# Performance work log

Hardware: AMD Instinct MI355X
Metric: run time of the kernel (lower is better)

Reference implementation:

```python
import jax, jax.numpy as jnp
import numpy as np

NUM_HEADS = 4
KERNEL = 4
EPS = 1e-6


def _causal_conv1d(x, w, b):
    # x: (B,S,D), w: (D,1,K) depthwise, b: (D,)
    xc = x.transpose(0, 2, 1)  # (B,D,S)
    y = jax.lax.conv_general_dilated(
        xc, w, window_strides=(1,), padding=[(w.shape[-1] - 1, 0)],
        feature_group_count=xc.shape[1])
    return (y + b[None, :, None]).transpose(0, 2, 1)  # (B,S,D)


def _headwise(x, w):
    # x: (B,S,D), w: (NH, DH_out, DH_in) block-diagonal linear, no bias
    B, S, D = x.shape
    nh, dout, din = w.shape
    xh = x.reshape(B, S, nh, din)
    return jnp.einsum('bshd,hod->bsho', xh, w).reshape(B, S, nh * dout)


def _slstm_scan(gates, R, b):
    # gates: (B,S,4,NH,DH) ordered [i,f,z,o]; R: (NH,DH,4*DH); b: (4,NH,DH)
    B, S, _, nh, dh = gates.shape
    gseq = gates.transpose(1, 0, 2, 3, 4)  # (S,B,4,NH,DH)
    zero = jnp.zeros((B, nh, dh), gates.dtype)
    init = (zero, zero, zero, zero)  # h, c, n, m

    def step(carry, g):
        h, c, n, m = carry
        rec = jnp.einsum('bhd,hdk->bhk', h, R)
        rec = rec.reshape(B, nh, 4, dh).transpose(0, 2, 1, 3)  # (B,4,NH,DH)
        raw = g + rec + b[None]
        iraw, fraw, zraw, oraw = raw[:, 0], raw[:, 1], raw[:, 2], raw[:, 3]
        logfplusm = m + jax.nn.log_sigmoid(fraw)
        m_new = jnp.maximum(iraw, logfplusm)  # stabilizer
        ig = jnp.exp(iraw - m_new)
        fg = jnp.exp(logfplusm - m_new)
        c_new = fg * c + ig * jnp.tanh(zraw)
        n_new = fg * n + ig
        h_new = jax.nn.sigmoid(oraw) * c_new / n_new
        return (h_new, c_new, n_new, m_new), h_new

    _, ys = jax.lax.scan(step, init, gseq)  # ys: (S,B,NH,DH)
    return ys.transpose(1, 2, 0, 3)  # (B,NH,S,DH)


def _multihead_layernorm(y, scale, bias):
    # y: (B,NH,S,DH); normalize over DH per head
    mu = y.mean(-1, keepdims=True)
    var = y.var(-1, keepdims=True)
    yn = (y - mu) * jax.lax.rsqrt(var + EPS)
    nh, dh = y.shape[1], y.shape[3]
    return yn * scale.reshape(1, nh, 1, dh) + bias.reshape(1, nh, 1, dh)


def setup_inputs() -> dict:
    key = jax.random.key(0)
    ks = jax.random.split(key, 12)
    B, S, D = 4, 2048, 1024
    nh, dh = NUM_HEADS, D // NUM_HEADS
    sd_conv = 1.0 / np.sqrt(KERNEL)
    sd_head = 1.0 / np.sqrt(dh)
    return {
        'x': jax.random.normal(ks[0], (B, S, D), jnp.float32),
        'conv_w': jax.random.normal(ks[1], (D, 1, KERNEL), jnp.float32) * sd_conv,
        'conv_b': jnp.zeros((D,), jnp.float32),
        'w_i': jax.random.normal(ks[2], (nh, dh, dh), jnp.float32) * sd_head,
        'w_f': jax.random.normal(ks[3], (nh, dh, dh), jnp.float32) * sd_head,
        'w_z': jax.random.normal(ks[4], (nh, dh, dh), jnp.float32) * sd_head,
        'w_o': jax.random.normal(ks[5], (nh, dh, dh), jnp.float32) * sd_head,
        'rec_kernel': jax.random.normal(ks[6], (nh, dh, 4 * dh), jnp.float32) * sd_head,
        'cell_bias': jnp.zeros((4, nh, dh), jnp.float32),
        'gn_scale': jnp.ones((D,), jnp.float32),
        'gn_bias': jnp.zeros((D,), jnp.float32),
    }


def reference(x, conv_w, conv_b, w_i, w_f, w_z, w_o, rec_kernel, cell_bias, gn_scale, gn_bias):
    B, S, D = x.shape
    dh = D // NUM_HEADS
    x_conv = jax.nn.swish(_causal_conv1d(x, conv_w, conv_b))
    i = _headwise(x_conv, w_i)
    f = _headwise(x_conv, w_f)
    z = _headwise(x, w_z)
    o = _headwise(x, w_o)
    # concat order [i,f,z,o]; reshape to (B,S,4,NH,DH)
    gates = jnp.stack([i, f, z, o], axis=2).reshape(B, S, 4, NUM_HEADS, dh)
    y = _slstm_scan(gates, rec_kernel, cell_bias)  # (B,NH,S,DH)
    out = _multihead_layernorm(y, gn_scale, gn_bias)
    return out.transpose(0, 2, 1, 3).reshape(B, S, D)
```

## Files before the change

### kernel.cpp

```cpp
#include <hip/hip_runtime.h>
#include <hip/hip_bf16.h>

#define NH 4
#define DH 256
#define DMODEL 1024
#define BB 4
#define SS 2048

typedef __attribute__((ext_vector_type(4))) float f32x4;
typedef __attribute__((ext_vector_type(8))) short bf16x8;
typedef __attribute__((ext_vector_type(4))) int i32x4;

__device__ __forceinline__ int dot4i8(int acc, int a, int b) {
#if __has_builtin(__builtin_amdgcn_sdot4)
    return __builtin_amdgcn_sdot4(a, b, acc, false);
#else
#pragma unroll
    for (int i = 0; i < 4; ++i) {
        int av = (a << (24 - 8 * i)) >> 24;
        int bv = (b << (24 - 8 * i)) >> 24;
        acc += av * bv;
    }
    return acc;
#endif
}

__device__ __forceinline__ void wg_barrier() {
    asm volatile("s_waitcnt lgkmcnt(0)" ::: "memory");
    __builtin_amdgcn_s_barrier();
}

__device__ __forceinline__ float xor1_f32(float v) {
    int r = __builtin_amdgcn_update_dpp(0, __float_as_int(v), 0xB1, 0xF, 0xF, true);
    return __int_as_float(r);
}

__global__ void k_conv(const float* __restrict__ x, const float* __restrict__ cw,
                       const float* __restrict__ cb, float* __restrict__ xc) {
    int bs = blockIdx.x;
    int s = bs & (SS - 1);
    const float* xrow = x + (size_t)bs * DMODEL;
#pragma unroll
    for (int dd = 0; dd < 4; ++dd) {
        int d = threadIdx.x + dd * 256;
        float w0 = cw[d * 4 + 0], w1 = cw[d * 4 + 1], w2 = cw[d * 4 + 2], w3 = cw[d * 4 + 3];
        float acc = cb[d] + w3 * xrow[d];
        if (s >= 1) acc += w2 * xrow[d - DMODEL];
        if (s >= 2) acc += w1 * xrow[d - 2 * DMODEL];
        if (s >= 3) acc += w0 * xrow[d - 3 * DMODEL];
        float sig = 1.f / (1.f + __expf(-acc));
        xc[(size_t)bs * DMODEL + d] = acc * sig;
    }
}

__global__ void k_gemm(const float* __restrict__ x, const float* __restrict__ xc,
                       const float* __restrict__ wi, const float* __restrict__ wf,
                       const float* __restrict__ wz, const float* __restrict__ wo,
                       float* __restrict__ gates) {
    int h = blockIdx.z >> 1, pair = blockIdx.z & 1;
    const float* A = pair ? x : xc;
    int n0 = blockIdx.y * 64;
    const float* W = (n0 < 256) ? (pair ? wz : wi) : (pair ? wo : wf);
    int nl = n0 & 255;
    int m0 = blockIdx.x * 64;

    __shared__ __align__(16) __hip_bfloat16 Al[64][72];
    __shared__ __align__(16) __hip_bfloat16 Bl[64][72];

    int tid = threadIdx.x;
    int lane = tid & 63, wv = tid >> 6;
    f32x4 acc[4] = {};

    for (int k0 = 0; k0 < 256; k0 += 64) {
        __syncthreads();
#pragma unroll
        for (int i = 0; i < 4; ++i) {
            int f4 = tid + i * 256;
            int r = f4 >> 4, c4 = (f4 & 15) * 4;
            const float* srcA = A + (size_t)(m0 + r) * DMODEL + h * DH + k0 + c4;
            float4 v = *(const float4*)srcA;
            Al[r][c4 + 0] = __float2bfloat16(v.x);
            Al[r][c4 + 1] = __float2bfloat16(v.y);
            Al[r][c4 + 2] = __float2bfloat16(v.z);
            Al[r][c4 + 3] = __float2bfloat16(v.w);
            const float* srcB = W + (size_t)(h * DH + nl + r) * DH + k0 + c4;
            float4 u = *(const float4*)srcB;
            Bl[r][c4 + 0] = __float2bfloat16(u.x);
            Bl[r][c4 + 1] = __float2bfloat16(u.y);
            Bl[r][c4 + 2] = __float2bfloat16(u.z);
            Bl[r][c4 + 3] = __float2bfloat16(u.w);
        }
        __syncthreads();
#pragma unroll
        for (int kk = 0; kk < 64; kk += 32) {
            bf16x8 a = *(const bf16x8*)&Al[wv * 16 + (lane & 15)][kk + (lane >> 4) * 8];
#pragma unroll
            for (int nt = 0; nt < 4; ++nt) {
                bf16x8 bfr = *(const bf16x8*)&Bl[nt * 16 + (lane & 15)][kk + (lane >> 4) * 8];
                acc[nt] = __builtin_amdgcn_mfma_f32_16x16x32_bf16(a, bfr, acc[nt], 0, 0, 0);
            }
        }
    }
#pragma unroll
    for (int nt = 0; nt < 4; ++nt)
#pragma unroll
        for (int r = 0; r < 4; ++r) {
            int m = m0 + wv * 16 + (lane >> 4) * 4 + r;
            int n = n0 + nt * 16 + (lane & 15);
            int b = m >> 11, s = m & (SS - 1);
            int g = pair * 2 + (n >> 8), d = n & 255;
            gates[((((size_t)(b * NH + h)) * SS + s) * 4 + g) * DH + d] = acc[nt][r];
        }
}

__global__ void k_prep(const float* __restrict__ R, int* __restrict__ Wq,
                       float* __restrict__ scales) {
    int colid = blockIdx.x * 4 + (threadIdx.x >> 6);
    int lane = threadIdx.x & 63;
    int h = colid >> 10, k = colid & 1023;
    const float* base = R + (size_t)h * 256 * 1024 + k;
    float v[4];
    float mx = 0.f;
#pragma unroll
    for (int i = 0; i < 4; ++i) {
        v[i] = base[(size_t)(lane * 4 + i) * 1024];
        mx = fmaxf(mx, fabsf(v[i]));
    }
    for (int off = 32; off; off >>= 1) mx = fmaxf(mx, __shfl_xor(mx, off));
    mx = fmaxf(mx, 1e-30f);
    float scale = mx * (1.f / 127.f);
    float inv = 127.f / mx;
    int pk = 0;
#pragma unroll
    for (int i = 0; i < 4; ++i) {
        int q = (int)rintf(v[i] * inv);
        q = max(-127, min(127, q));
        pk |= (q & 255) << (8 * i);
    }
    Wq[(h * 64 + lane) * 1024 + k] = pk;
    if (lane == 0) scales[h * 1024 + k] = scale;
}

__launch_bounds__(512, 2)
__global__ void k_scan(const float* __restrict__ gates, const int* __restrict__ Wq,
                       const float* __restrict__ scales, const float* __restrict__ bias,
                       float* __restrict__ y) {
    int bh = blockIdx.x;
    int h = bh & 3;
    int t = threadIdx.x;
    int d = t >> 1, pair = t & 1;

    __shared__ __align__(16) signed char hq[2][256];

    int col0 = pair * 256 + d;
    int col1 = col0 + 512;

    int w0[64], w1[64];
#pragma unroll
    for (int j = 0; j < 64; ++j) {
        w0[j] = Wq[(h * 64 + j) * 1024 + col0];
        w1[j] = Wq[(h * 64 + j) * 1024 + col1];
    }
    float cm0 = scales[h * 1024 + col0] * (1.f / 127.f);
    float cm1 = scales[h * 1024 + col1] * (1.f / 127.f);
    float b0 = bias[(pair * NH + h) * DH + d];
    float b1 = bias[((2 + pair) * NH + h) * DH + d];

    float c = 0.f, n = 0.f, mstate = 0.f;
    const float* gbase = gates + (size_t)bh * SS * 1024;
    float* ybase = y + (size_t)bh * SS * DH + d;

    if (t < 32) ((i32x4*)hq)[t] = (i32x4){0, 0, 0, 0};
    __syncthreads();

    float gA0 = gbase[col0], gA1 = gbase[col1];
    float gB0 = gbase[1024 + col0], gB1 = gbase[1024 + col1];

#define SCAN_STEP(P, G0, G1, SCUR)                                            \
    {                                                                          \
        int acc0 = 0, acc1 = 0;                                                \
        const i32x4* hv4 = (const i32x4*)hq[P];                                \
        _Pragma("unroll") for (int kb = 0; kb < 4; ++kb) {                     \
            i32x4 ha = hv4[kb * 4 + 0];                                        \
            i32x4 hb = hv4[kb * 4 + 1];                                        \
            i32x4 hc = hv4[kb * 4 + 2];                                        \
            i32x4 hd_ = hv4[kb * 4 + 3];                                       \
            int hd[16] = {ha.x, ha.y, ha.z, ha.w, hb.x, hb.y, hb.z, hb.w,      \
                          hc.x, hc.y, hc.z, hc.w, hd_.x, hd_.y, hd_.z, hd_.w}; \
            _Pragma("unroll") for (int j = 0; j < 16; ++j) {                   \
                acc0 = dot4i8(acc0, w0[kb * 16 + j], hd[j]);                   \
                acc1 = dot4i8(acc1, w1[kb * 16 + j], hd[j]);                   \
            }                                                                  \
        }                                                                      \
        float rawA = G0 + (float)acc0 * cm0 + b0;                              \
        float rawB = G1 + (float)acc1 * cm1 + b1;                              \
        int sp = (SCUR) + 2 < SS ? (SCUR) + 2 : SS - 1;                        \
        G0 = gbase[(size_t)sp * 1024 + col0];                                  \
        G1 = gbase[(size_t)sp * 1024 + col1];                                  \
        float recvA = xor1_f32(rawA);                                          \
        float recvB = xor1_f32(rawB);                                          \
        float rawi = pair ? recvA : rawA;                                      \
        float rawf = pair ? rawA : recvA;                                      \
        float rawz = pair ? recvB : rawB;                                      \
        float rawo = pair ? rawB : recvB;                                      \
        float lsf = fminf(rawf, 0.f) - __logf(1.f + __expf(-fabsf(rawf)));     \
        float lfm = mstate + lsf;                                              \
        float mn = fmaxf(rawi, lfm);                                           \
        float ig = __expf(rawi - mn);                                          \
        float fg = __expf(lfm - mn);                                           \
        float az = fabsf(rawz);                                                \
        float e2 = __expf(-2.f * az);                                          \
        float th = (1.f - e2) / (1.f + e2);                                    \
        th = rawz < 0.f ? -th : th;                                            \
        c = fg * c + ig * th;                                                  \
        n = fg * n + ig;                                                       \
        mstate = mn;                                                           \
        float so = 1.f / (1.f + __expf(-rawo));                                \
        float hv = so * c / n;                                                 \
        if (!pair) {                                                           \
            ybase[(size_t)(SCUR)*DH] = hv;                                     \
            hq[(P) ^ 1][d] = (signed char)(int)rintf(hv * 127.f);              \
        }                                                                      \
        wg_barrier();                                                          \
    }

    for (int s = 0; s < SS; s += 2) {
        SCAN_STEP(0, gA0, gA1, s)
        SCAN_STEP(1, gB0, gB1, s + 1)
    }
#undef SCAN_STEP
}

__global__ void k_ln(const float* __restrict__ y, const float* __restrict__ gsc,
                     const float* __restrict__ gbi, float* __restrict__ out) {
    int bid = blockIdx.x;
    int s = bid & (SS - 1);
    int bh = bid >> 11;
    int b = bh >> 2, h = bh & 3;
    int d = threadIdx.x;
    float v = y[(size_t)bid * DH + d];
    float s1 = v, s2 = v * v;
    for (int off = 32; off; off >>= 1) {
        s1 += __shfl_xor(s1, off);
        s2 += __shfl_xor(s2, off);
    }
    __shared__ float a1[4], a2[4];
    int wv = threadIdx.x >> 6, ln = threadIdx.x & 63;
    if (ln == 0) { a1[wv] = s1; a2[wv] = s2; }
    __syncthreads();
    s1 = a1[0] + a1[1] + a1[2] + a1[3];
    s2 = a2[0] + a2[1] + a2[2] + a2[3];
    float mu = s1 * (1.f / 256.f);
    float var = s2 * (1.f / 256.f) - mu * mu;
    float rs = rsqrtf(var + 1e-6f);
    float o = (v - mu) * rs * gsc[h * DH + d] + gbi[h * DH + d];
    out[((size_t)(b * SS + s)) * DMODEL + h * DH + d] = o;
}

extern "C" void kernel_launch(void* const* d_in, const int* in_sizes, int n_in,
                              void* d_out, int out_size, void* d_ws, size_t ws_size,
                              hipStream_t stream) {
    (void)in_sizes; (void)n_in; (void)out_size; (void)ws_size;
    const float* x = (const float*)d_in[0];
    const float* cw = (const float*)d_in[1];
    const float* cb = (const float*)d_in[2];
    const float* wi = (const float*)d_in[3];
    const float* wf = (const float*)d_in[4];
    const float* wz = (const float*)d_in[5];
    const float* wo = (const float*)d_in[6];
    const float* R = (const float*)d_in[7];
    const float* cbias = (const float*)d_in[8];
    const float* gsc = (const float*)d_in[9];
    const float* gbi = (const float*)d_in[10];
    float* out = (float*)d_out;

    char* ws = (char*)d_ws;
    float* xc = (float*)ws;
    float* gates = (float*)(ws + 33554432ull);
    float* yb = (float*)(ws + 167772160ull);
    int* Wq = (int*)(ws + 201326592ull);
    float* scales = (float*)(ws + 202375168ull);

    k_prep<<<1024, 256, 0, stream>>>(R, Wq, scales);
    k_conv<<<BB * SS, 256, 0, stream>>>(x, cw, cb, xc);
    k_gemm<<<dim3(128, 8, 8), 256, 0, stream>>>(x, xc, wi, wf, wz, wo, gates);
    k_scan<<<16, 512, 0, stream>>>(gates, Wq, scales, cbias, yb);
    k_ln<<<BB * SS * NH, 256, 0, stream>>>(yb, gsc, gbi, out);
}
```

Measured before the change: 2.136 ms.

## Split scan recurrence between MFMA for input gate and sdot4 for others

The scan kernel moves from 512 threads (two per hidden unit, exchanging gate values via DPP) to 256 threads, one per hidden unit. The input-gate recurrent matvec now runs on the int8 MFMA unit with its result broadcast by lane shuffles, while the forget, z and output gates stay on scalar sdot4 loops held in registers. The aim is to overlap matrix-core and VALU work inside each sequential step and drop the pair exchange. The cost is higher register pressure per thread and a heavier VALU chain per lane, which could lengthen each step.

```diff
diff --git a/kernel.cpp b/kernel.cpp
--- a/kernel.cpp
+++ b/kernel.cpp
@@ -28,11 +28,7 @@
 __device__ __forceinline__ void wg_barrier() {
     asm volatile("s_waitcnt lgkmcnt(0)" ::: "memory");
     __builtin_amdgcn_s_barrier();
-}
-
-__device__ __forceinline__ float xor1_f32(float v) {
-    int r = __builtin_amdgcn_update_dpp(0, __float_as_int(v), 0xB1, 0xF, 0xF, true);
-    return __int_as_float(r);
+    __builtin_amdgcn_sched_barrier(0);
 }
 
 __global__ void k_conv(const float* __restrict__ x, const float* __restrict__ cw,
@@ -141,94 +137,137 @@
     if (lane == 0) scales[h * 1024 + k] = scale;
 }
 
-__launch_bounds__(512, 2)
+__launch_bounds__(256, 1)
 __global__ void k_scan(const float* __restrict__ gates, const int* __restrict__ Wq,
                        const float* __restrict__ scales, const float* __restrict__ bias,
                        float* __restrict__ y) {
     int bh = blockIdx.x;
     int h = bh & 3;
-    int t = threadIdx.x;
-    int d = t >> 1, pair = t & 1;
+    int d = threadIdx.x;
+    int lane = d & 63;
+    int wv = d >> 6;
+    int kg = lane >> 4;
+    int cl = lane & 15;
 
     __shared__ __align__(16) signed char hq[2][256];
 
-    int col0 = pair * 256 + d;
-    int col1 = col0 + 512;
-
-    int w0[64], w1[64];
+    int wf[64], wz[64], wo[64];
 #pragma unroll
     for (int j = 0; j < 64; ++j) {
-        w0[j] = Wq[(h * 64 + j) * 1024 + col0];
-        w1[j] = Wq[(h * 64 + j) * 1024 + col1];
-    }
-    float cm0 = scales[h * 1024 + col0] * (1.f / 127.f);
-    float cm1 = scales[h * 1024 + col1] * (1.f / 127.f);
-    float b0 = bias[(pair * NH + h) * DH + d];
-    float b1 = bias[((2 + pair) * NH + h) * DH + d];
-
-    float c = 0.f, n = 0.f, mstate = 0.f;
+        const int* row = Wq + (size_t)(h * 64 + j) * 1024 + d;
+        wf[j] = row[256];
+        wz[j] = row[512];
+        wo[j] = row[768];
+    }
+
+    i32x4 bfr[4][4];
+#pragma unroll
+    for (int tt = 0; tt < 4; ++tt) {
+        int col = wv * 64 + tt * 16 + cl;
+#pragma unroll
+        for (int c = 0; c < 4; ++c)
+#pragma unroll
+            for (int j4 = 0; j4 < 4; ++j4)
+                bfr[tt][c][j4] = Wq[(h * 64 + c * 16 + kg * 4 + j4) * 1024 + col];
+    }
+    i32x4 acc[4];
+#pragma unroll
+    for (int tt = 0; tt < 4; ++tt) acc[tt] = (i32x4){0, 0, 0, 0};
+
+    float cmi = scales[h * 1024 + d] * (1.f / 127.f);
+    float cmf = scales[h * 1024 + 256 + d] * (1.f / 127.f);
+    float cmz = scales[h * 1024 + 512 + d] * (1.f / 127.f);
+    float cmo = scales[h * 1024 + 768 + d] * (1.f / 127.f);
+    float bi = bias[(0 * NH + h) * DH + d];
+    float bf_ = bias[(1 * NH + h) * DH + d];
+    float bz = bias[(2 * NH + h) * DH + d];
+    float bo = bias[(3 * NH + h) * DH + d];
+
+    float c_ = 0.f, n_ = 0.f, mstate = 0.f;
     const float* gbase = gates + (size_t)bh * SS * 1024;
-    float* ybase = y + (size_t)bh * SS * DH + d;
-
-    if (t < 32) ((i32x4*)hq)[t] = (i32x4){0, 0, 0, 0};
+    float* ybase = y + (size_t)bh * SS * DH;
+
+    if (d < 32) ((i32x4*)hq)[d] = (i32x4){0, 0, 0, 0};
     __syncthreads();
 
-    float gA0 = gbase[col0], gA1 = gbase[col1];
-    float gB0 = gbase[1024 + col0], gB1 = gbase[1024 + col1];
-
-#define SCAN_STEP(P, G0, G1, SCUR)                                            \
+    float gA0 = gbase[d], gA1 = gbase[256 + d], gA2 = gbase[512 + d], gA3 = gbase[768 + d];
+    float gB0 = gbase[1024 + d], gB1 = gbase[1024 + 256 + d];
+    float gB2 = gbase[1024 + 512 + d], gB3 = gbase[1024 + 768 + d];
+
+#define DOT3(JJ, HV)                  \
+    af = dot4i8(af, wf[JJ], (HV));    \
+    az = dot4i8(az, wz[JJ], (HV));    \
+    ao = dot4i8(ao, wo[JJ], (HV));
+
+#define SCAN_STEP(P, G0, G1, G2, G3, SCUR)                                     \
     {                                                                          \
-        int acc0 = 0, acc1 = 0;                                                \
-        const i32x4* hv4 = (const i32x4*)hq[P];                                \
-        _Pragma("unroll") for (int kb = 0; kb < 4; ++kb) {                     \
-            i32x4 ha = hv4[kb * 4 + 0];                                        \
-            i32x4 hb = hv4[kb * 4 + 1];                                        \
-            i32x4 hc = hv4[kb * 4 + 2];                                        \
-            i32x4 hd_ = hv4[kb * 4 + 3];                                       \
-            int hd[16] = {ha.x, ha.y, ha.z, ha.w, hb.x, hb.y, hb.z, hb.w,      \
-                          hc.x, hc.y, hc.z, hc.w, hd_.x, hd_.y, hd_.z, hd_.w}; \
-            _Pragma("unroll") for (int j = 0; j < 16; ++j) {                   \
-                acc0 = dot4i8(acc0, w0[kb * 16 + j], hd[j]);                   \
-                acc1 = dot4i8(acc1, w1[kb * 16 + j], hd[j]);                   \
-            }                                                                  \
+        int sp = (SCUR) + 2 < SS ? (SCUR) + 2 : SS - 1;                        \
+        const float* gp = gbase + (size_t)sp * 1024 + d;                       \
+        float p0 = gp[0], p1 = gp[256], p2 = gp[512], p3 = gp[768];            \
+        const i32x4* hp = (const i32x4*)hq[P];                                 \
+                                    \
+        i32x4 a0 = hp[kg], a1 = hp[4 + kg], a2 = hp[8 + kg], a3 = hp[12 + kg]; \
+        acc[0].x = 0; acc[1].x = 0; acc[2].x = 0; acc[3].x = 0;                \
+        _Pragma("unroll") for (int tt = 0; tt < 4; ++tt)                       \
+            acc[tt] = __builtin_amdgcn_mfma_i32_16x16x64_i8(a0, bfr[tt][0], acc[tt], 0, 0, 0); \
+        _Pragma("unroll") for (int tt = 0; tt < 4; ++tt)                       \
+            acc[tt] = __builtin_amdgcn_mfma_i32_16x16x64_i8(a1, bfr[tt][1], acc[tt], 0, 0, 0); \
+        _Pragma("unroll") for (int tt = 0; tt < 4; ++tt)                       \
+            acc[tt] = __builtin_amdgcn_mfma_i32_16x16x64_i8(a2, bfr[tt][2], acc[tt], 0, 0, 0); \
+        _Pragma("unroll") for (int tt = 0; tt < 4; ++tt)                       \
+            acc[tt] = __builtin_amdgcn_mfma_i32_16x16x64_i8(a3, bfr[tt][3], acc[tt], 0, 0, 0); \
+                 \
+        int af = 0, az = 0, ao = 0;                                            \
+        _Pragma("unroll") for (int cc = 0; cc < 4; ++cc) {                     \
+            i32x4 h0 = hp[cc * 4 + 0], h1 = hp[cc * 4 + 1];                    \
+            i32x4 h2 = hp[cc * 4 + 2], h3 = hp[cc * 4 + 3];                    \
+            DOT3(cc * 16 + 0, h0.x)  DOT3(cc * 16 + 1, h0.y)                   \
+            DOT3(cc * 16 + 2, h0.z)  DOT3(cc * 16 + 3, h0.w)                   \
+            DOT3(cc * 16 + 4, h1.x)  DOT3(cc * 16 + 5, h1.y)                   \
+            DOT3(cc * 16 + 6, h1.z)  DOT3(cc * 16 + 7, h1.w)                   \
+            DOT3(cc * 16 + 8, h2.x)  DOT3(cc * 16 + 9, h2.y)                   \
+            DOT3(cc * 16 + 10, h2.z) DOT3(cc * 16 + 11, h2.w)                  \
+            DOT3(cc * 16 + 12, h3.x) DOT3(cc * 16 + 13, h3.y)                  \
+            DOT3(cc * 16 + 14, h3.z) DOT3(cc * 16 + 15, h3.w)                  \
         }                                                                      \
-        float rawA = G0 + (float)acc0 * cm0 + b0;                              \
-        float rawB = G1 + (float)acc1 * cm1 + b1;                              \
-        int sp = (SCUR) + 2 < SS ? (SCUR) + 2 : SS - 1;                        \
-        G0 = gbase[(size_t)sp * 1024 + col0];                                  \
-        G1 = gbase[(size_t)sp * 1024 + col1];                                  \
-        float recvA = xor1_f32(rawA);                                          \
-        float recvB = xor1_f32(rawB);                                          \
-        float rawi = pair ? recvA : rawA;                                      \
-        float rawf = pair ? rawA : recvA;                                      \
-        float rawz = pair ? recvB : rawB;                                      \
-        float rawo = pair ? rawB : recvB;                                      \
+               \
+        int s0 = __shfl(acc[0].x, cl);                                         \
+        int s1 = __shfl(acc[1].x, cl);                                         \
+        int s2 = __shfl(acc[2].x, cl);                                         \
+        int s3 = __shfl(acc[3].x, cl);                                         \
+        int v01 = (d & 16) ? s1 : s0;                                          \
+        int v23 = (d & 16) ? s3 : s2;                                          \
+        int ri_raw = (d & 32) ? v23 : v01;                                     \
+        float rawi = (G0) + (float)ri_raw * cmi + bi;                          \
+        float rawf = (G1) + (float)af * cmf + bf_;                             \
+        float rawz = (G2) + (float)az * cmz + bz;                              \
+        float rawo = (G3) + (float)ao * cmo + bo;                              \
         float lsf = fminf(rawf, 0.f) - __logf(1.f + __expf(-fabsf(rawf)));     \
         float lfm = mstate + lsf;                                              \
         float mn = fmaxf(rawi, lfm);                                           \
         float ig = __expf(rawi - mn);                                          \
         float fg = __expf(lfm - mn);                                           \
-        float az = fabsf(rawz);                                                \
-        float e2 = __expf(-2.f * az);                                          \
+        float az_ = fabsf(rawz);                                               \
+        float e2 = __expf(-2.f * az_);                                         \
         float th = (1.f - e2) / (1.f + e2);                                    \
         th = rawz < 0.f ? -th : th;                                            \
-        c = fg * c + ig * th;                                                  \
-        n = fg * n + ig;                                                       \
+        c_ = fg * c_ + ig * th;                                                \
+        n_ = fg * n_ + ig;                                                     \
         mstate = mn;                                                           \
         float so = 1.f / (1.f + __expf(-rawo));                                \
-        float hv = so * c / n;                                                 \
-        if (!pair) {                                                           \
-            ybase[(size_t)(SCUR)*DH] = hv;                                     \
-            hq[(P) ^ 1][d] = (signed char)(int)rintf(hv * 127.f);              \
-        }                                                                      \
+        float hv = so * c_ / n_;                                               \
+        ybase[(size_t)(SCUR)*DH + d] = hv;                                     \
+        hq[(P) ^ 1][d] = (signed char)(int)rintf(hv * 127.f);                  \
+        G0 = p0; G1 = p1; G2 = p2; G3 = p3;                                    \
         wg_barrier();                                                          \
     }
 
     for (int s = 0; s < SS; s += 2) {
-        SCAN_STEP(0, gA0, gA1, s)
-        SCAN_STEP(1, gB0, gB1, s + 1)
+        SCAN_STEP(0, gA0, gA1, gA2, gA3, s)
+        SCAN_STEP(1, gB0, gB1, gB2, gB3, s + 1)
     }
 #undef SCAN_STEP
+#undef DOT3
 }
 
 __global__ void k_ln(const float* __restrict__ y, const float* __restrict__ gsc,
@@ -284,6 +323,6 @@
     k_prep<<<1024, 256, 0, stream>>>(R, Wq, scales);
     k_conv<<<BB * SS, 256, 0, stream>>>(x, cw, cb, xc);
     k_gemm<<<dim3(128, 8, 8), 256, 0, stream>>>(x, xc, wi, wf, wz, wo, gates);
-    k_scan<<<16, 512, 0, stream>>>(gates, Wq, scales, cbias, yb);
+    k_scan<<<16, 256, 0, stream>>>(gates, Wq, scales, cbias, yb);
     k_ln<<<BB * SS * NH, 256, 0, stream>>>(yb, gsc, gbi, out);
 }
```

Result: slower. 2.304 ms (+7.8%).
